# Optimization experiments

Hardware: AMD Instinct MI355X
Metric: run time of the kernel (lower is better)

The kernel has to match this reference:

```python
import jax, jax.numpy as jnp
import numpy as np

B, S, H, I, E, K = 4, 2048, 1024, 4096, 8, 2


def setup_inputs() -> dict:
    key = jax.random.key(0)
    ks = jax.random.split(key, 6)
    x = jax.random.normal(ks[0], (B, S, H), dtype=jnp.float32)
    gate_w = jax.random.normal(ks[1], (H, E), dtype=jnp.float32) * 0.02
    up_w = jax.random.normal(ks[2], (E, H, I), dtype=jnp.float32) * 0.02
    up_b = jnp.zeros((E, I), dtype=jnp.float32)
    down_w = jax.random.normal(ks[3], (E, I, H), dtype=jnp.float32) * 0.02
    down_b = jnp.zeros((E, H), dtype=jnp.float32)
    return {"x": x, "gate_w": gate_w, "up_w": up_w, "up_b": up_b,
            "down_w": down_w, "down_b": down_b}


def reference(x, gate_w, up_w, up_b, down_w, down_b):
    # Router: logits [B,S,E], softmax probs
    logits = jnp.einsum('bsh,he->bse', x, gate_w)
    probs = jax.nn.softmax(logits, axis=-1)
    # top-k selection and renormalization of the selected probabilities
    topk_p, topk_idx = jax.lax.top_k(probs, K)            # [B,S,K]
    topk_p = topk_p / jnp.sum(topk_p, axis=-1, keepdims=True)
    # combine weights per expert: [B,S,E] (sum of renormalized top-k probs routed to e)
    combine = jnp.sum(jax.nn.one_hot(topk_idx, E, dtype=x.dtype) * topk_p[..., None], axis=2)
    # per-expert FFN, weighted combine (loop over fixed small expert set)
    out = jnp.zeros_like(x)
    for e in range(E):
        h = jax.nn.gelu(jnp.einsum('bsh,hi->bsi', x, up_w[e]) + up_b[e], approximate=False)
        y = jnp.einsum('bsi,ih->bsh', h, down_w[e]) + down_b[e]
        out = out + combine[..., e:e + 1] * y
    # aux statistics
    expert_usage = jnp.mean(probs, axis=(0, 1))           # [E]
    load_balance_loss = E * jnp.sum(expert_usage * expert_usage)
    top_expert = topk_idx[..., 0]                          # [B,S]
    return out, load_balance_loss, expert_usage, top_expert
```

## Files before the change

### kernel.cpp

```cpp
#include <hip/hip_runtime.h>
#include <cmath>

#define T_TOK 8192
#define HDIM 1024
#define IDIM 4096
#define NEXP 8

#define OFF_LOSS  8388608
#define OFF_USAGE 8388609
#define OFF_TOPE  8388617

typedef __attribute__((ext_vector_type(8))) short bf16x8;
typedef __attribute__((ext_vector_type(4))) float f32x4;
typedef unsigned short u16;
typedef unsigned int u32;

__device__ inline u16 f2bf(float f) {
  u32 u = __float_as_uint(f);
  u32 r = (u + 0x7FFFu + ((u >> 16) & 1u)) >> 16;
  return (u16)r;
}

__device__ inline void glds16(const void* g, void* l) {
  __builtin_amdgcn_global_load_lds(
      (const __attribute__((address_space(1))) u32*)g,
      (__attribute__((address_space(3))) u32*)l, 16, 0, 0);
}

__global__ __launch_bounds__(256)
void cvt_x(const float* __restrict__ x, u16* __restrict__ xb) {
  size_t i = ((size_t)blockIdx.x * 256 + threadIdx.x) * 8;
  float4 a = *(const float4*)(x + i);
  float4 b = *(const float4*)(x + i + 4);
  union { u16 s[8]; uint4 v; } u;
  u.s[0] = f2bf(a.x); u.s[1] = f2bf(a.y); u.s[2] = f2bf(a.z); u.s[3] = f2bf(a.w);
  u.s[4] = f2bf(b.x); u.s[5] = f2bf(b.y); u.s[6] = f2bf(b.z); u.s[7] = f2bf(b.w);
  *(uint4*)(xb + i) = u.v;
}

__global__ __launch_bounds__(256)
void transpose_cvt64(const float* __restrict__ src, u16* __restrict__ dst, int R, int C) {
  __shared__ float tile[64][65];
  size_t eoff = (size_t)blockIdx.z * R * C;
  int r0 = blockIdx.y * 64, c0 = blockIdx.x * 64;
  const float* s = src + eoff;
  u16* d = dst + eoff;
  int tr = threadIdx.x >> 4;
  int tc = (threadIdx.x & 15) * 4;
#pragma unroll
  for (int it = 0; it < 4; it++) {
    int row = tr + it * 16;
    float4 v = *(const float4*)(s + (size_t)(r0 + row) * C + c0 + tc);
    tile[row][tc] = v.x; tile[row][tc + 1] = v.y;
    tile[row][tc + 2] = v.z; tile[row][tc + 3] = v.w;
  }
  __syncthreads();
  int wc = threadIdx.x >> 3;
  int wr = (threadIdx.x & 7) * 8;
#pragma unroll
  for (int it = 0; it < 2; it++) {
    int c = wc + it * 32;
    union { u16 s[8]; uint4 v; } u;
#pragma unroll
    for (int j = 0; j < 8; j++) u.s[j] = f2bf(tile[wr + j][c]);
    *(uint4*)(d + (size_t)(c0 + c) * R + r0 + wr) = u.v;
  }
}

__global__ __launch_bounds__(256)
void router_kernel(const float* __restrict__ x, const float* __restrict__ gw,
                   float* __restrict__ probs, int* __restrict__ counts,
                   int* __restrict__ tlist, float* __restrict__ wlist,
                   float* __restrict__ out) {
  int wid = threadIdx.x >> 6, lane = threadIdx.x & 63;
  int tok = blockIdx.x * 4 + wid;
  double acc[NEXP];
#pragma unroll
  for (int e = 0; e < NEXP; e++) acc[e] = 0.0;
  const float* xr = x + (size_t)tok * HDIM;
  for (int h = lane; h < HDIM; h += 64) {
    double xv = (double)xr[h];
    const float* g = gw + h * NEXP;
#pragma unroll
    for (int e = 0; e < NEXP; e++) acc[e] += xv * (double)g[e];
  }
#pragma unroll
  for (int off = 32; off > 0; off >>= 1) {
#pragma unroll
    for (int e = 0; e < NEXP; e++) acc[e] += __shfl_xor(acc[e], off);
  }
  if (lane == 0) {
    double m = acc[0];
#pragma unroll
    for (int e = 1; e < NEXP; e++) if (acc[e] > m) m = acc[e];
    double p[NEXP], ssum = 0.0;
#pragma unroll
    for (int e = 0; e < NEXP; e++) { p[e] = exp(acc[e] - m); ssum += p[e]; }
#pragma unroll
    for (int e = 0; e < NEXP; e++) p[e] /= ssum;
    int i1 = 0;
#pragma unroll
    for (int e = 1; e < NEXP; e++) if (p[e] > p[i1]) i1 = e;
    int i2 = (i1 == 0) ? 1 : 0;
#pragma unroll
    for (int e = 0; e < NEXP; e++) if (e != i1 && p[e] > p[i2]) i2 = e;
    double ps = p[i1] + p[i2];
#pragma unroll
    for (int e = 0; e < NEXP; e++) probs[(size_t)tok * NEXP + e] = (float)p[e];
    out[OFF_TOPE + tok] = (float)i1;
    int pos1 = atomicAdd(&counts[i1], 1);
    tlist[i1 * T_TOK + pos1] = tok;
    wlist[i1 * T_TOK + pos1] = (float)(p[i1] / ps);
    int pos2 = atomicAdd(&counts[i2], 1);
    tlist[i2 * T_TOK + pos2] = tok;
    wlist[i2 * T_TOK + pos2] = (float)(p[i2] / ps);
  }
}

__global__ void hbase_kernel(const int* __restrict__ counts, int* __restrict__ hbase) {
  if (threadIdx.x == 0 && blockIdx.x == 0) {
    int s = 0;
    for (int e = 0; e < NEXP; e++) { hbase[e] = s; s += counts[e]; }
    hbase[NEXP] = s;
  }
}

__global__ __launch_bounds__(256)
void usage_kernel(const float* __restrict__ probs, float* __restrict__ out) {
  int e = blockIdx.x;
  float s = 0.f;
  for (int t = threadIdx.x; t < T_TOK; t += 256) s += probs[(size_t)t * NEXP + e];
#pragma unroll
  for (int off = 32; off > 0; off >>= 1) s += __shfl_xor(s, off);
  __shared__ float red[4];
  int lane = threadIdx.x & 63, wid = threadIdx.x >> 6;
  if (lane == 0) red[wid] = s;
  __syncthreads();
  if (threadIdx.x == 0)
    out[OFF_USAGE + e] = (red[0] + red[1] + red[2] + red[3]) / (float)T_TOK;
}

__global__ void loss_kernel(float* __restrict__ out) {
  if (threadIdx.x == 0 && blockIdx.x == 0) {
    float s = 0.f;
    for (int e = 0; e < NEXP; e++) { float u = out[OFF_USAGE + e]; s += u * u; }
    out[OFF_LOSS] = (float)NEXP * s;
  }
}


#define STAGE(Ts, kk)                                                        \
  do {                                                                       \
    int cs_ = (Ts) & 1;                                                      \
    u32 kof_ = (u32)(Ts) * 64 + (kk) * 32;                                   \
    u16* Ld_ = lds + cs_ * 32768 + (kk) * 8192;                              \
    glds16(pa0 + kof_, Ld_ + t * 8);                                         \
    glds16(pa1 + kof_, Ld_ + 4096 + t * 8);                                  \
    glds16(pb0 + kof_, Ld_ + 16384 + t * 8);                                 \
    glds16(pb1 + kof_, Ld_ + 16384 + 4096 + t * 8);                          \
  } while (0)

#define COMPUTE_HALF(c, kk)                                                  \
  do {                                                                       \
    const u16* Ld_ = lds + (c) * 32768 + (kk) * 8192;                        \
    bf16x8 bf_[4], af_[8];                                                   \
    _Pragma("unroll") for (int ni = 0; ni < 4; ni++) {                       \
      int rb = wc * 64 + ni * 16 + lrow;                                     \
      bf_[ni] = *(const bf16x8*)&Ld_[16384 + rb * 32 +                       \
                                     ((lslot ^ (rb & 3)) * 8)];              \
    }                                                                        \
    _Pragma("unroll") for (int mi = 0; mi < 8; mi++) {                       \
      int r = wr * 128 + mi * 16 + lrow;                                     \
      af_[mi] = *(const bf16x8*)&Ld_[r * 32 + ((lslot ^ (r & 3)) * 8)];      \
    }                                                                        \
    __builtin_amdgcn_s_setprio(1);                                           \
    _Pragma("unroll") for (int mi = 0; mi < 8; mi++)                         \
    _Pragma("unroll") for (int ni = 0; ni < 4; ni++)                         \
      acc[mi][ni] = __builtin_amdgcn_mfma_f32_16x16x32_bf16(                 \
          af_[mi], bf_[ni], acc[mi][ni], 0, 0, 0);                           \
    __builtin_amdgcn_s_setprio(0);                                           \
  } while (0)

#define GEMM_KLOOP(nt)                                                       \
  STAGE(0, 0); STAGE(0, 1); STAGE(1, 0);                                     \
  _Pragma("unroll 2") for (int T = 0; T < (nt); ++T) {                       \
    int c = T & 1;                                                           \
    if (T == (nt) - 1) asm volatile("s_waitcnt vmcnt(4)" ::: "memory");      \
    else               asm volatile("s_waitcnt vmcnt(8)" ::: "memory");      \
    __builtin_amdgcn_s_barrier();                                            \
    asm volatile("" ::: "memory");                                           \
    if (T + 1 < (nt)) STAGE(T + 1, 1);                                       \
    COMPUTE_HALF(c, 0);                                                      \
    if (T == (nt) - 1) asm volatile("s_waitcnt vmcnt(0)" ::: "memory");      \
    else               asm volatile("s_waitcnt vmcnt(8)" ::: "memory");      \
    __builtin_amdgcn_s_barrier();                                            \
    asm volatile("" ::: "memory");                                           \
    if (T + 2 < (nt)) STAGE(T + 2, 0);                                       \
    COMPUTE_HALF(c, 1);                                                      \
  }

#define GEMM_COMMON                                                          \
  int t = threadIdx.x;                                                       \
  int lane = t & 63, wid = t >> 6;                                           \
  int lrow = lane & 15, lslot = lane >> 4;                                   \
  int wr = wid >> 2, wc = wid & 3;                                           \
  int rA = t >> 2;                                                           \
  int skA = (t & 3) ^ (rA & 3);                                              \
  f32x4 acc[8][4];                                                           \
  _Pragma("unroll") for (int i = 0; i < 8; i++)                              \
  _Pragma("unroll") for (int j = 0; j < 4; j++)                              \
      acc[i][j] = (f32x4){0.f, 0.f, 0.f, 0.f};

__global__ __launch_bounds__(512, 2)
void up_gemm(const u16* __restrict__ xb, const u16* __restrict__ wbt,
             const float* __restrict__ bias, const int* __restrict__ counts,
             const int* __restrict__ hbase, const int* __restrict__ tlist,
             u16* __restrict__ hout, int e_fixed) {
  const int NT = IDIM / 256;
  const int MT = T_TOK / 256;
  int q = gridDim.x >> 3;
  int orig = blockIdx.x;
  int wg = (orig & 7) * q + (orig >> 3);
  int e, tm, tn;
  if (e_fixed >= 0) { e = e_fixed; tm = wg / NT; tn = wg % NT; }
  else { e = wg / (MT * NT); int r = wg % (MT * NT); tm = r / NT; tn = r % NT; }
  int cnt = counts[e];
  int m0 = tm * 256;
  if (m0 >= cnt) return;
  int hb = (e_fixed >= 0) ? 0 : hbase[e];
  int n0 = tn * 256;

  __shared__ u16 lds[65536];

  GEMM_COMMON

  const int* tl = tlist + e * T_TOK;
  int g0 = m0 + rA;       if (g0 > cnt - 1) g0 = cnt - 1;
  int g1 = m0 + 128 + rA; if (g1 > cnt - 1) g1 = cnt - 1;
  const u16* pa0 = xb + (size_t)tl[g0] * HDIM + skA * 8;
  const u16* pa1 = xb + (size_t)tl[g1] * HDIM + skA * 8;
  const u16* wb = wbt + (size_t)e * IDIM * HDIM;
  const u16* pb0 = wb + (size_t)(n0 + rA) * HDIM + skA * 8;
  const u16* pb1 = wb + (size_t)(n0 + 128 + rA) * HDIM + skA * 8;

  GEMM_KLOOP(HDIM / 64)

  float bv[4];
#pragma unroll
  for (int ni = 0; ni < 4; ni++)
    bv[ni] = bias[(size_t)e * IDIM + n0 + wc * 64 + ni * 16 + lrow];
  int r4 = lslot * 4;
#pragma unroll
  for (int mi = 0; mi < 8; mi++) {
    int rb = m0 + wr * 128 + mi * 16 + r4;
#pragma unroll
    for (int j = 0; j < 4; j++) {
      int row = rb + j;
      if (row < cnt) {
        u16* hp = hout + (size_t)(hb + row) * IDIM + n0 + wc * 64 + lrow;
#pragma unroll
        for (int ni = 0; ni < 4; ni++) {
          float v = acc[mi][ni][j] + bv[ni];
          float gl = 0.5f * v * (1.0f + erff(v * 0.70710678118654752f));
          hp[ni * 16] = f2bf(gl);
        }
      }
    }
  }
}

__global__ __launch_bounds__(512, 2)
void down_gemm(const u16* __restrict__ h, const u16* __restrict__ wbt,
               const float* __restrict__ bias, const int* __restrict__ counts,
               const int* __restrict__ hbase, const int* __restrict__ tlist,
               const float* __restrict__ wlist, float* __restrict__ out, int e_fixed) {
  const int NT = HDIM / 256;
  const int MT = T_TOK / 256;
  const int KS = 2;
  int q = gridDim.x >> 3;
  int orig = blockIdx.x;
  int wg = (orig & 7) * q + (orig >> 3);
  int e, r;
  if (e_fixed >= 0) { e = e_fixed; r = wg; }
  else { e = wg / (MT * NT * KS); r = wg % (MT * NT * KS); }
  int tm = r / (NT * KS);
  int r2 = r % (NT * KS);
  int ks = r2 / NT;
  int tn = r2 % NT;
  int cnt = counts[e];
  int m0 = tm * 256;
  if (m0 >= cnt) return;
  int hb = (e_fixed >= 0) ? 0 : hbase[e];
  int n0 = tn * 256;
  int kbase = ks * (IDIM / KS);

  __shared__ u16 lds[65536];

  GEMM_COMMON

  int g0 = m0 + rA;       if (g0 > cnt - 1) g0 = cnt - 1;
  int g1 = m0 + 128 + rA; if (g1 > cnt - 1) g1 = cnt - 1;
  const u16* pa0 = h + (size_t)(hb + g0) * IDIM + kbase + skA * 8;
  const u16* pa1 = h + (size_t)(hb + g1) * IDIM + kbase + skA * 8;
  const u16* wb = wbt + (size_t)e * HDIM * IDIM;
  const u16* pb0 = wb + (size_t)(n0 + rA) * IDIM + kbase + skA * 8;
  const u16* pb1 = wb + (size_t)(n0 + 128 + rA) * IDIM + kbase + skA * 8;

  GEMM_KLOOP((IDIM / KS) / 64)

  float bv[4];
#pragma unroll
  for (int ni = 0; ni < 4; ni++)
    bv[ni] = (ks == 0) ? bias[(size_t)e * HDIM + n0 + wc * 64 + ni * 16 + lrow] : 0.0f;
  int r4 = lslot * 4;
#pragma unroll
  for (int mi = 0; mi < 8; mi++) {
    int rb = m0 + wr * 128 + mi * 16 + r4;
#pragma unroll
    for (int j = 0; j < 4; j++) {
      int row = rb + j;
      if (row < cnt) {
        int tok = tlist[e * T_TOK + row];
        float w = wlist[e * T_TOK + row];
        float* op = out + (size_t)tok * HDIM + n0 + wc * 64 + lrow;
#pragma unroll
        for (int ni = 0; ni < 4; ni++)
          atomicAdd(&op[ni * 16], w * (acc[mi][ni][j] + bv[ni]));
      }
    }
  }
}

extern "C" void kernel_launch(void* const* d_in, const int* in_sizes, int n_in,
                              void* d_out, int out_size, void* d_ws, size_t ws_size,
                              hipStream_t stream) {
  const float* x   = (const float*)d_in[0];
  const float* gw  = (const float*)d_in[1];
  const float* upw = (const float*)d_in[2];
  const float* upb = (const float*)d_in[3];
  const float* dnw = (const float*)d_in[4];
  const float* dnb = (const float*)d_in[5];
  float* out = (float*)d_out;
  char* ws = (char*)d_ws;

  int*   counts = (int*)(ws + 0);
  int*   hbase  = (int*)(ws + 64);
  int*   tlist  = (int*)(ws + 256);
  float* wlist  = (float*)(ws + 256 + 262144);
  float* probs  = (float*)(ws + 256 + 2 * 262144);
  u16*   xb     = (u16*)(ws + 1048576);
  u16*   upbt   = (u16*)(ws + 1048576 + 16777216);
  u16*   dnbt   = (u16*)(ws + 1048576 + 16777216 + 67108864ull);
  u16*   hbuf   = (u16*)(ws + 1048576 + 16777216 + 2ull * 67108864ull);

  bool grouped = ws_size >= 286261248ull;

  hipMemsetAsync(counts, 0, 32, stream);
  hipMemsetAsync(d_out, 0, (size_t)out_size * 4, stream);

  cvt_x<<<4096, 256, 0, stream>>>(x, xb);
  transpose_cvt64<<<dim3(IDIM / 64, HDIM / 64, NEXP), 256, 0, stream>>>(upw, upbt, HDIM, IDIM);
  transpose_cvt64<<<dim3(HDIM / 64, IDIM / 64, NEXP), 256, 0, stream>>>(dnw, dnbt, IDIM, HDIM);
  router_kernel<<<T_TOK / 4, 256, 0, stream>>>(x, gw, probs, counts, tlist, wlist, out);
  hbase_kernel<<<1, 64, 0, stream>>>(counts, hbase);
  usage_kernel<<<NEXP, 256, 0, stream>>>(probs, out);
  loss_kernel<<<1, 64, 0, stream>>>(out);

  if (grouped) {
    up_gemm<<<NEXP * 32 * 16, 512, 0, stream>>>(xb, upbt, upb, counts, hbase, tlist, hbuf, -1);
    down_gemm<<<NEXP * 32 * 4 * 2, 512, 0, stream>>>(hbuf, dnbt, dnb, counts, hbase, tlist, wlist, out, -1);
  } else {
    for (int e = 0; e < NEXP; e++) {
      up_gemm<<<32 * 16, 512, 0, stream>>>(xb, upbt, upb, counts, hbase, tlist, hbuf, e);
      down_gemm<<<32 * 4 * 2, 512, 0, stream>>>(hbuf, dnbt, dnb, counts, hbase, tlist, wlist, out, e);
    }
  }
}
```

Before: 831.3 us.

## Split GEMM k-step into ping-pong LDS-read/MFMA phases and change LDS swizzle

Restructures the GEMM k-loop so each half-tile is processed in two smaller phases: read B plus the low A rows, run 16 MFMAs, then read the high A rows and run 16 more, with barriers between phases so waves interleave LDS reads and matrix work. It also changes the LDS XOR swizzle from row&3 to (row>>1)&3, applied on both the writer side (skA) and the reader side, to reduce bank conflicts. This lowers register pressure for A fragments and aims for better overlap, at the cost of many more barriers per iteration. Correctness depends on the vmcnt accounting remaining valid for the new barrier placement.

```diff
diff --git a/kernel.cpp b/kernel.cpp
--- a/kernel.cpp
+++ b/kernel.cpp
@@ -160,43 +160,72 @@
     glds16(pb1 + kof_, Ld_ + 16384 + 4096 + t * 8);                          \
   } while (0)
 
-#define COMPUTE_HALF(c, kk)                                                  \
-  do {                                                                       \
-    const u16* Ld_ = lds + (c) * 32768 + (kk) * 8192;                        \
-    bf16x8 bf_[4], af_[8];                                                   \
-    _Pragma("unroll") for (int ni = 0; ni < 4; ni++) {                       \
-      int rb = wc * 64 + ni * 16 + lrow;                                     \
-      bf_[ni] = *(const bf16x8*)&Ld_[16384 + rb * 32 +                       \
-                                     ((lslot ^ (rb & 3)) * 8)];              \
-    }                                                                        \
-    _Pragma("unroll") for (int mi = 0; mi < 8; mi++) {                       \
-      int r = wr * 128 + mi * 16 + lrow;                                     \
-      af_[mi] = *(const bf16x8*)&Ld_[r * 32 + ((lslot ^ (r & 3)) * 8)];      \
-    }                                                                        \
-    __builtin_amdgcn_s_setprio(1);                                           \
-    _Pragma("unroll") for (int mi = 0; mi < 8; mi++)                         \
-    _Pragma("unroll") for (int ni = 0; ni < 4; ni++)                         \
-      acc[mi][ni] = __builtin_amdgcn_mfma_f32_16x16x32_bf16(                 \
-          af_[mi], bf_[ni], acc[mi][ni], 0, 0, 0);                           \
-    __builtin_amdgcn_s_setprio(0);                                           \
-  } while (0)
+#define RD_B(Lp)                                                             \
+  _Pragma("unroll") for (int ni = 0; ni < 4; ni++) {                         \
+    int rb_ = wc * 64 + ni * 16 + lrow;                                      \
+    bf_[ni] = *(const bf16x8*)&(Lp)[16384 + rb_ * 32 +                       \
+                                    ((lslot ^ ((rb_ >> 1) & 3)) * 8)];       \
+  }
+
+#define RD_ALO(Lp)                                                           \
+  _Pragma("unroll") for (int mi = 0; mi < 4; mi++) {                         \
+    int r_ = wr * 128 + mi * 16 + lrow;                                      \
+    af_[mi] = *(const bf16x8*)&(Lp)[r_ * 32 + ((lslot ^ ((r_ >> 1) & 3)) * 8)];\
+  }
+
+#define RD_AHI(Lp)                                                           \
+  _Pragma("unroll") for (int mi = 0; mi < 4; mi++) {                         \
+    int r_ = wr * 128 + 64 + mi * 16 + lrow;                                 \
+    af_[mi] = *(const bf16x8*)&(Lp)[r_ * 32 + ((lslot ^ ((r_ >> 1) & 3)) * 8)];\
+  }
+
+#define MFMA16(base)                                                         \
+  __builtin_amdgcn_s_setprio(1);                                             \
+  _Pragma("unroll") for (int mi = 0; mi < 4; mi++)                           \
+  _Pragma("unroll") for (int ni = 0; ni < 4; ni++)                           \
+    acc[(base) + mi][ni] = __builtin_amdgcn_mfma_f32_16x16x32_bf16(          \
+        af_[mi], bf_[ni], acc[(base) + mi][ni], 0, 0, 0);                    \
+  __builtin_amdgcn_s_setprio(0);
 
 #define GEMM_KLOOP(nt)                                                       \
   STAGE(0, 0); STAGE(0, 1); STAGE(1, 0);                                     \
+  asm volatile("s_waitcnt vmcnt(8)" ::: "memory");                           \
+  __builtin_amdgcn_s_barrier();                                              \
   _Pragma("unroll 2") for (int T = 0; T < (nt); ++T) {                       \
-    int c = T & 1;                                                           \
-    if (T == (nt) - 1) asm volatile("s_waitcnt vmcnt(4)" ::: "memory");      \
-    else               asm volatile("s_waitcnt vmcnt(8)" ::: "memory");      \
-    __builtin_amdgcn_s_barrier();                                            \
-    asm volatile("" ::: "memory");                                           \
+    int c_ = T & 1;                                                          \
+    const u16* L0_ = lds + c_ * 32768;                                       \
+    const u16* L1_ = lds + c_ * 32768 + 8192;                                \
+    bf16x8 bf_[4], af_[4];                                                   \
+                                                                    \
+    RD_B(L0_); RD_ALO(L0_);                                                  \
     if (T + 1 < (nt)) STAGE(T + 1, 1);                                       \
-    COMPUTE_HALF(c, 0);                                                      \
+    __builtin_amdgcn_s_barrier();                                            \
+    asm volatile("s_waitcnt lgkmcnt(0)" ::: "memory");                       \
+    MFMA16(0);                                                               \
+    __builtin_amdgcn_s_barrier();                                            \
+                                                                    \
+    RD_AHI(L0_);                                                             \
+    __builtin_amdgcn_s_barrier();                                            \
+    asm volatile("s_waitcnt lgkmcnt(0)" ::: "memory");                       \
+    MFMA16(4);                                                               \
     if (T == (nt) - 1) asm volatile("s_waitcnt vmcnt(0)" ::: "memory");      \
     else               asm volatile("s_waitcnt vmcnt(8)" ::: "memory");      \
     __builtin_amdgcn_s_barrier();                                            \
-    asm volatile("" ::: "memory");                                           \
+                                                                    \
+    RD_B(L1_); RD_ALO(L1_);                                                  \
     if (T + 2 < (nt)) STAGE(T + 2, 0);                                       \
-    COMPUTE_HALF(c, 1);                                                      \
+    __builtin_amdgcn_s_barrier();                                            \
+    asm volatile("s_waitcnt lgkmcnt(0)" ::: "memory");                       \
+    MFMA16(0);                                                               \
+    __builtin_amdgcn_s_barrier();                                            \
+                                                                    \
+    RD_AHI(L1_);                                                             \
+    __builtin_amdgcn_s_barrier();                                            \
+    asm volatile("s_waitcnt lgkmcnt(0)" ::: "memory");                       \
+    MFMA16(4);                                                               \
+    if (T == (nt) - 1) asm volatile("s_waitcnt vmcnt(0)" ::: "memory");      \
+    else               asm volatile("s_waitcnt vmcnt(8)" ::: "memory");      \
+    __builtin_amdgcn_s_barrier();                                            \
   }
 
 #define GEMM_COMMON                                                          \
@@ -205,7 +234,7 @@
   int lrow = lane & 15, lslot = lane >> 4;                                   \
   int wr = wid >> 2, wc = wid & 3;                                           \
   int rA = t >> 2;                                                           \
-  int skA = (t & 3) ^ (rA & 3);                                              \
+  int skA = (t & 3) ^ ((rA >> 1) & 3);                                       \
   f32x4 acc[8][4];                                                           \
   _Pragma("unroll") for (int i = 0; i < 8; i++)                              \
   _Pragma("unroll") for (int j = 0; j < 4; j++)                              \
```

Result: no change. 844.8 us (+1.6%).
